# Optimization experiments

Measured on AMD Instinct MI355X. Metric: run time of the kernel, lower is better.

Reference implementation:

```python
import jax, jax.numpy as jnp
import numpy as np

N_EMBD = 2048
N_HEAD = 32
N_GROUPS = 8
HEAD_DIM = N_EMBD // N_HEAD
Q_PER_KV = N_HEAD // N_GROUPS
QKV_DIM = (Q_PER_KV + 2) * N_GROUPS * HEAD_DIM


def apply_rope(x, cos, sin):
    # x: [B, nH, T, hd]; cos/sin: [T, rot//2]
    B, nH, T, hd = x.shape
    rot = min(sin.shape[1] * 2, hd)
    half = rot // 2
    x_rot, x_pass = x[..., :rot], x[..., rot:]
    c = cos[:T, :half][None, None]  # [1,1,T,half]
    s = sin[:T, :half][None, None]
    x1, x2 = x_rot[..., :half], x_rot[..., half:]
    x1_ = x1 * c - x2 * s
    x2_ = x2 * c + x1 * s
    return jnp.concatenate([x1_, x2_, x_pass], axis=-1)


def setup_inputs() -> dict:
    key = jax.random.key(0)
    k1, k2, k3, k4, k5 = jax.random.split(key, 5)
    B, T = 2, 2048
    x = jax.random.normal(k1, (B, T, N_EMBD), dtype=jnp.float32)
    cos = jax.random.uniform(k2, (T, HEAD_DIM // 2), dtype=jnp.float32)
    sin = jax.random.uniform(k3, (T, HEAD_DIM // 2), dtype=jnp.float32)
    attn_w = jax.random.normal(k4, (QKV_DIM, N_EMBD), dtype=jnp.float32) * (1.0 / np.sqrt(N_EMBD))
    proj_w = jax.random.normal(k5, (N_EMBD, N_EMBD), dtype=jnp.float32) * (1.0 / np.sqrt(N_EMBD))
    return {"x": x, "cos": cos, "sin": sin, "attn_w": attn_w, "proj_w": proj_w}


def reference(x, cos, sin, attn_w, proj_w):
    B, T, E = x.shape
    qkv = jnp.einsum('bte,fe->btf', x, attn_w)  # [B,T,QKV_DIM]
    qkv = qkv.reshape(B, T, N_GROUPS, Q_PER_KV + 2, HEAD_DIM)
    q = qkv[:, :, :, :Q_PER_KV].reshape(B, T, N_HEAD, HEAD_DIM)
    k = qkv[:, :, :, Q_PER_KV]      # [B,T,G,hd]
    v = qkv[:, :, :, Q_PER_KV + 1]  # [B,T,G,hd]
    # [B, heads, T, hd] layout; GQA repeat_interleave of K/V to full head count
    q = q.transpose(0, 2, 1, 3)
    k = jnp.repeat(k.transpose(0, 2, 1, 3), Q_PER_KV, axis=1)
    v = jnp.repeat(v.transpose(0, 2, 1, 3), Q_PER_KV, axis=1)
    q = apply_rope(q, cos, sin)
    k = apply_rope(k, cos, sin)
    scale = 1.0 / np.sqrt(HEAD_DIM)
    att = jax.nn.softmax(jnp.einsum('bhqd,bhkd->bhqk', q, k) * scale, axis=-1)
    out = jnp.einsum('bhqk,bhkd->bhqd', att, v)  # [B,nH,T,hd]
    out = out.transpose(0, 2, 1, 3).reshape(B, T, N_HEAD * HEAD_DIM)
    return jnp.einsum('bte,fe->btf', out, proj_w)
```

## Files before the change

### kernel.cpp

```cpp
#include <hip/hip_runtime.h>

typedef unsigned short u16;
typedef unsigned int u32;
typedef __bf16 bf16x8 __attribute__((ext_vector_type(8)));
typedef float f32x4 __attribute__((ext_vector_type(4)));
typedef float f32x16 __attribute__((ext_vector_type(16)));
typedef unsigned int u32x4 __attribute__((ext_vector_type(4)));

__device__ __forceinline__ u16 f2bf(float f) {
    u32 u = __builtin_bit_cast(u32, f);
    u32 r = u + 0x7FFFu + ((u >> 16) & 1u);
    return (u16)(r >> 16);
}
__device__ __forceinline__ u32 pack_bf16(float v0, float v1) {
    u32 a = __builtin_bit_cast(u32, v0) + 0x8000u;
    u32 b = __builtin_bit_cast(u32, v1) + 0x8000u;
    return __builtin_amdgcn_perm(b, a, 0x07060302u);
}
__device__ __forceinline__ u32 cvtpk(float lo, float hi) {
    u32 r;
    asm("v_cvt_pk_bf16_f32 %0, %1, %2" : "=v"(r) : "v"(lo), "v"(hi));
    return r;
}
__device__ __forceinline__ void plswap(u32& a, u32& b) {
    asm("v_permlane32_swap_b32 %0, %1" : "+v"(a), "+v"(b));
}
__device__ __forceinline__ void gload16(const u16* g, u16* l) {
    __builtin_amdgcn_global_load_lds(
        (const __attribute__((address_space(1))) u32*)g,
        (__attribute__((address_space(3))) u32*)l, 16, 0, 0);
}

#define QSCALE 0.18033688011111793f


__global__ __launch_bounds__(256) void cvt3_kernel(const float* __restrict__ a, u16* __restrict__ ao,
                                                   const float* __restrict__ b, u16* __restrict__ bo,
                                                   const float* __restrict__ c, u16* __restrict__ co) {
    int i = blockIdx.x * 256 + threadIdx.x;
    const float* src; u16* dst; int idx;
    if (i < 2097152)       { src = a; dst = ao; idx = i; }
    else if (i < 3670016)  { src = b; dst = bo; idx = i - 2097152; }
    else                   { src = c; dst = co; idx = i - 3670016; }
    float4 f = reinterpret_cast<const float4*>(src)[idx];
    u32 lo = (u32)f2bf(f.x) | ((u32)f2bf(f.y) << 16);
    u32 hi = (u32)f2bf(f.z) | ((u32)f2bf(f.w) << 16);
    reinterpret_cast<uint2*>(dst)[idx] = make_uint2(lo, hi);
}

__global__ __launch_bounds__(512, 2) void gemm_qkv(const u16* __restrict__ A,
                                                   const u16* __restrict__ Bw,
                                                   const float* __restrict__ cosb,
                                                   const float* __restrict__ sinb,
                                                   u16* __restrict__ Qo,
                                                   u16* __restrict__ Ko,
                                                   u16* __restrict__ Vt) {
    __shared__ __align__(16) u16 As[2 * 2 * 128 * 64];
    __shared__ __align__(16) u16 Bs[2 * 2 * 128 * 64];
    const int tid = threadIdx.x;
    const int w = tid >> 6, lane = tid & 63;
    const int quad = lane >> 4, l15 = lane & 15;
    const int wr = w >> 2, wc = w & 3;
    const int m0 = blockIdx.x * 256, n0 = blockIdx.y * 256;
    const int K = 2048;
    const int rsub = lane >> 3;
    const int csrc = (lane & 7) ^ rsub;
    const int sx = (l15 & 7) << 3;
    const int c0 = (quad * 8) ^ sx;
    const int c1 = (32 + quad * 8) ^ sx;

    f32x4 acc[8][4];
#pragma unroll
    for (int a = 0; a < 8; a++)
#pragma unroll
        for (int b = 0; b < 4; b++) acc[a][b] = (f32x4){0.f, 0.f, 0.f, 0.f};

    auto stage = [&](const u16* g, int row0, int kk, u16* lds) {
#pragma unroll
        for (int i = 0; i < 2; i++)
            gload16(g + (size_t)(row0 + (i * 8 + w) * 8 + rsub) * K + kk + csrc * 8,
                    lds + (i * 8 + w) * 512);
    };

    stage(A,  m0,       0, &As[0]);
    stage(A,  m0 + 128, 0, &As[8192]);
    stage(Bw, n0,       0, &Bs[0]);
    stage(Bw, n0 + 128, 0, &Bs[8192]);
    asm volatile("s_waitcnt vmcnt(0)" ::: "memory");
    __builtin_amdgcn_s_barrier();

    for (int j = 0; j < 32; ++j) {
        const int cur = j & 1;
        const u16* Ab = &As[cur * 16384 + wr * 8192];
        const u16* Bb = &Bs[cur * 16384 + (wc >> 1) * 8192 + (wc & 1) * 4096];
        u16* Asn = &As[(cur ^ 1) * 16384];
        u16* Bsn = &Bs[(cur ^ 1) * 16384];
        const int kk2 = (j + 1) * 64;
        bf16x8 af[4][2];
#pragma unroll
        for (int q = 0; q < 4; ++q) {
            const int qm = q >> 1, qn = q & 1;
            if (qn == 0) {
#pragma unroll
                for (int fm = 0; fm < 4; fm++) {
                    af[fm][0] = *reinterpret_cast<const bf16x8*>(&Ab[(qm * 64 + fm * 16 + l15) * 64 + c0]);
                    af[fm][1] = *reinterpret_cast<const bf16x8*>(&Ab[(qm * 64 + fm * 16 + l15) * 64 + c1]);
                }
            }
            bf16x8 bfv[2][2];
#pragma unroll
            for (int fn = 0; fn < 2; fn++) {
                bfv[fn][0] = *reinterpret_cast<const bf16x8*>(&Bb[(qn * 32 + fn * 16 + l15) * 64 + c0]);
                bfv[fn][1] = *reinterpret_cast<const bf16x8*>(&Bb[(qn * 32 + fn * 16 + l15) * 64 + c1]);
            }
            if (j < 31) {
                if (q == 0)      { stage(A,  m0,       kk2, Asn); stage(A,  m0 + 128, kk2, Asn + 8192); }
                else if (q == 1) { stage(Bw, n0,       kk2, Bsn); stage(Bw, n0 + 128, kk2, Bsn + 8192); }
            }
            __builtin_amdgcn_s_barrier();
            __builtin_amdgcn_s_setprio(1);
#pragma unroll
            for (int fm = 0; fm < 4; fm++)
#pragma unroll
                for (int fn = 0; fn < 2; fn++) {
                    acc[qm * 4 + fm][qn * 2 + fn] = __builtin_amdgcn_mfma_f32_16x16x32_bf16(
                        af[fm][0], bfv[fn][0], acc[qm * 4 + fm][qn * 2 + fn], 0, 0, 0);
                    acc[qm * 4 + fm][qn * 2 + fn] = __builtin_amdgcn_mfma_f32_16x16x32_bf16(
                        af[fm][1], bfv[fn][1], acc[qm * 4 + fm][qn * 2 + fn], 0, 0, 0);
                }
            __builtin_amdgcn_s_setprio(0);
            if (q == 3 && j < 31) asm volatile("s_waitcnt vmcnt(0)" ::: "memory");
            __builtin_amdgcn_s_barrier();
        }
    }

    const int nw0 = n0 + wc * 64;
    const int G = nw0 / 384;
    const int slot = (nw0 % 384) / 64;
    const int bb = m0 >> 11;
    const int tb0 = (m0 & 2047) + wr * 128 + quad * 4;
    if (slot == 5) {
        u16* vbase = Vt + ((size_t)(bb * 8 + G)) * 131072;
        const int half_v = quad >> 1, jb = (quad & 1) * 4;
#pragma unroll
        for (int fm = 0; fm < 8; fm++) {
            const int trow = tb0 + fm * 16;
            const int sb = (trow >> 6) * 4096 + ((trow >> 4) & 3) * 512 + half_v * 256 + jb;
#pragma unroll
            for (int fn = 0; fn < 4; fn++) {
                const int dt = fn >> 1, dl = (fn & 1) * 16 + l15;
                uint2 pk;
                pk.x = pack_bf16(acc[fm][fn][0], acc[fm][fn][1]);
                pk.y = pack_bf16(acc[fm][fn][2], acc[fm][fn][3]);
                *reinterpret_cast<uint2*>(vbase + sb + dt * 2048 + dl * 8) = pk;
            }
        }
    } else {
        const float sc = (slot < 4) ? QSCALE : 1.0f;
        u16* obase = (slot < 4)
            ? Qo + ((size_t)(bb * 32 + G * 4 + slot)) * 131072
            : Ko + ((size_t)(bb * 8 + G)) * 131072;
        const int laneoff = (l15 >> 3) * 256 + (l15 & 7);
#pragma unroll
        for (int fm = 0; fm < 8; fm++) {
#pragma unroll
            for (int i = 0; i < 4; i++) {
                const int t = tb0 + fm * 16 + i;
                const int tb = (t >> 5) * 2048 + (t & 31) * 8 + laneoff;
#pragma unroll
                for (int fn = 0; fn < 2; fn++) {
                    const int dh = fn * 16 + l15;
                    float c = cosb[t * 32 + dh], s = sinb[t * 32 + dh];
                    float x1 = acc[fm][fn][i], x2 = acc[fm][fn + 2][i];
                    obase[tb + fn * 512]       = f2bf((x1 * c - x2 * s) * sc);
                    obase[tb + (fn + 2) * 512] = f2bf((x2 * c + x1 * s) * sc);
                }
            }
        }
    }
}

__global__ __launch_bounds__(256) void gemm_bt(const u16* __restrict__ A,
                                               const u16* __restrict__ Bw,
                                               float* __restrict__ Cf,
                                               int M, int N, int K) {
    __shared__ __align__(16) u16 As[2 * 128 * 32];
    __shared__ __align__(16) u16 Bs[2 * 128 * 32];
    const int tid = threadIdx.x;
    const int wave = tid >> 6, lane = tid & 63, quad = lane >> 4, l15 = lane & 15;
    const int wm = wave >> 1, wn = wave & 1;
    const int m0 = blockIdx.x * 128, n0 = blockIdx.y * 128;
    const int lrow = lane >> 2, lcol = (lane & 3) * 8;
    f32x4 acc[4][4];
#pragma unroll
    for (int a = 0; a < 4; a++)
#pragma unroll
        for (int b = 0; b < 4; b++) acc[a][b] = (f32x4){0.f, 0.f, 0.f, 0.f};
    for (int kk = 0; kk < K; kk += 64) {
        __syncthreads();
#pragma unroll
        for (int p = 0; p < 2; p++)
#pragma unroll
            for (int c = 0; c < 2; c++) {
                const int rA = wave * 32 + c * 16;
                gload16(A  + (size_t)(m0 + rA + lrow) * K + kk + p * 32 + lcol,
                        &As[p * 4096 + rA * 32]);
                gload16(Bw + (size_t)(n0 + rA + lrow) * K + kk + p * 32 + lcol,
                        &Bs[p * 4096 + rA * 32]);
            }
        __syncthreads();
#pragma unroll
        for (int p = 0; p < 2; p++) {
            bf16x8 af[4], bfr[4];
#pragma unroll
            for (int t = 0; t < 4; t++) {
                af[t]  = *reinterpret_cast<const bf16x8*>(
                    &As[p * 4096 + (wm * 64 + t * 16 + l15) * 32 + quad * 8]);
                bfr[t] = *reinterpret_cast<const bf16x8*>(
                    &Bs[p * 4096 + (wn * 64 + t * 16 + l15) * 32 + quad * 8]);
            }
#pragma unroll
            for (int tm = 0; tm < 4; tm++)
#pragma unroll
                for (int tn = 0; tn < 4; tn++)
                    acc[tm][tn] = __builtin_amdgcn_mfma_f32_16x16x32_bf16(af[tm], bfr[tn], acc[tm][tn], 0, 0, 0);
        }
    }
#pragma unroll
    for (int tm = 0; tm < 4; tm++) {
        const int r0 = m0 + wm * 64 + tm * 16 + quad * 4;
#pragma unroll
        for (int tn = 0; tn < 4; tn++) {
            const int c = n0 + wn * 64 + tn * 16 + l15;
#pragma unroll
            for (int i = 0; i < 4; i++) Cf[(size_t)(r0 + i) * N + c] = acc[tm][tn][i];
        }
    }
}

__global__ __launch_bounds__(256, 4) void attn(const u16* __restrict__ Q,
                                               const u16* __restrict__ Kg,
                                               const u16* __restrict__ Vt,
                                               u16* __restrict__ O) {
    __shared__ __align__(16) u16 Ks[2 * 4096];
    __shared__ __align__(16) u16 Vts[2 * 4096];
    const int tid = threadIdx.x, w = tid >> 6, lane = tid & 63;
    const int half = lane >> 5, l31 = lane & 31;
    const int q0 = blockIdx.x * 128;
    const int h = blockIdx.y, b = blockIdx.z, g = h >> 2;
    const u16* qfb = Q + ((size_t)(b * 32 + h)) * 131072;
    const u16* kfb = Kg + ((size_t)(b * 8 + g)) * 131072;
    const u16* vfb = Vt + ((size_t)(b * 8 + g)) * 131072;

    const int Tq = (q0 >> 6) + (w >> 1);
#pragma unroll
    for (int ks = 0; ks < 4; ks++)
        gload16(qfb + ((size_t)((Tq * 8 + (w & 1) * 4 + ks) * 64) + lane) * 8,
                Ks + (w * 4 + ks) * 512);
    __syncthreads();
    bf16x8 qf[4];
#pragma unroll
    for (int ks = 0; ks < 4; ks++)
        qf[ks] = *reinterpret_cast<const bf16x8*>(&Ks[(w * 4 + ks) * 512 + lane * 8]);
    __syncthreads();

    f32x16 Oa[2];
#pragma unroll
    for (int t = 0; t < 2; t++)
#pragma unroll
        for (int i = 0; i < 16; i++) Oa[t][i] = 0.f;
    float lsum = 0.f;

    auto stage_kv = [&](int T, int bsel) {
        u16* kd = Ks + bsel * 4096;
        u16* vd = Vts + bsel * 4096;
#pragma unroll
        for (int i = 0; i < 2; i++) {
            const int s = w * 2 + i;
            gload16(kfb + ((size_t)((T * 8 + s) * 64) + lane) * 8, kd + s * 512);
            gload16(vfb + ((size_t)((T * 8 + s) * 64) + lane) * 8, vd + s * 512);
        }
    };

    stage_kv(0, 0);
    __syncthreads();

    for (int t = 0; t < 32; t++) {
        if (t < 31) stage_kv(t + 1, (t + 1) & 1);
        const u16* Kb = Ks + (t & 1) * 4096;
        const u16* Vb = Vts + (t & 1) * 4096;

        float ps = 0.f;
        u32 pw[4][4];
#pragma unroll
        for (int kt = 0; kt < 2; kt++) {
            f32x16 S;
#pragma unroll
            for (int i = 0; i < 16; i++) S[i] = 0.f;
            __builtin_amdgcn_s_setprio(1);
#pragma unroll
            for (int ks = 0; ks < 4; ks++) {
                bf16x8 kf = *reinterpret_cast<const bf16x8*>(
                    &Kb[(kt * 4 + ks) * 512 + lane * 8]);
                S = __builtin_amdgcn_mfma_f32_32x32x16_bf16(kf, qf[ks], S, 0, 0, 0);
            }
            __builtin_amdgcn_s_setprio(0);
            float pe[16];
#pragma unroll
            for (int r = 0; r < 16; r++) pe[r] = __builtin_amdgcn_exp2f(S[r]);
#pragma unroll
            for (int r = 0; r < 4; r++)
                ps += (pe[r * 4 + 0] + pe[r * 4 + 1]) + (pe[r * 4 + 2] + pe[r * 4 + 3]);
#pragma unroll
            for (int j = 0; j < 2; j++) {
                u32 X0 = cvtpk(pe[j * 8 + 0], pe[j * 8 + 1]);
                u32 Y0 = cvtpk(pe[j * 8 + 4], pe[j * 8 + 5]);
                u32 X1 = cvtpk(pe[j * 8 + 2], pe[j * 8 + 3]);
                u32 Y1 = cvtpk(pe[j * 8 + 6], pe[j * 8 + 7]);
                plswap(X0, Y0);
                plswap(X1, Y1);
                const int ks2 = kt * 2 + j;
                pw[ks2][0] = X0; pw[ks2][1] = X1; pw[ks2][2] = Y0; pw[ks2][3] = Y1;
            }
        }
        lsum += ps;
        __builtin_amdgcn_s_setprio(1);
#pragma unroll
        for (int ks2 = 0; ks2 < 4; ks2++) {
            u32x4 pv = (u32x4){pw[ks2][0], pw[ks2][1], pw[ks2][2], pw[ks2][3]};
            bf16x8 pf = __builtin_bit_cast(bf16x8, pv);
#pragma unroll
            for (int dt = 0; dt < 2; dt++) {
                bf16x8 vf = *reinterpret_cast<const bf16x8*>(
                    &Vb[(dt * 4 + ks2) * 512 + lane * 8]);
                Oa[dt] = __builtin_amdgcn_mfma_f32_32x32x16_bf16(vf, pf, Oa[dt], 0, 0, 0);
            }
        }
        __builtin_amdgcn_s_setprio(0);
        __syncthreads();
    }
    float lt = lsum + __shfl_xor(lsum, 32);
    float linv = 1.f / lt;
    const int t = q0 + w * 32 + l31;
    u16* orow = O + ((size_t)(b * 2048 + t)) * 2048 + h * 64;
#pragma unroll
    for (int dt = 0; dt < 2; dt++)
#pragma unroll
        for (int gr = 0; gr < 4; gr++) {
            uint2 pk;
            pk.x = pack_bf16(Oa[dt][gr * 4 + 0] * linv, Oa[dt][gr * 4 + 1] * linv);
            pk.y = pack_bf16(Oa[dt][gr * 4 + 2] * linv, Oa[dt][gr * 4 + 3] * linv);
            *reinterpret_cast<uint2*>(orow + dt * 32 + 8 * gr + 4 * half) = pk;
        }
}

extern "C" void kernel_launch(void* const* d_in, const int* in_sizes, int n_in,
                              void* d_out, int out_size, void* d_ws, size_t ws_size,
                              hipStream_t stream) {
    const float* x      = (const float*)d_in[0];
    const float* cosb   = (const float*)d_in[1];
    const float* sinb   = (const float*)d_in[2];
    const float* attn_w = (const float*)d_in[3];
    const float* proj_w = (const float*)d_in[4];
    float* out = (float*)d_out;

    u16* xb  = (u16*)d_ws;
    u16* w1b = xb  + (size_t)4096 * 2048;
    u16* w2b = w1b + (size_t)3072 * 2048;
    u16* qo  = w2b + (size_t)2048 * 2048;
    u16* ko  = qo  + (size_t)2 * 32 * 2048 * 64;
    u16* vt  = ko  + (size_t)2 * 8 * 2048 * 64;
    u16* ao  = xb;

    cvt3_kernel<<<18432, 256, 0, stream>>>(x, xb, attn_w, w1b, proj_w, w2b);
    gemm_qkv<<<dim3(16, 12), 512, 0, stream>>>(xb, w1b, cosb, sinb, qo, ko, vt);
    attn<<<dim3(16, 32, 2), 256, 0, stream>>>(qo, ko, vt, ao);
    gemm_bt<<<dim3(32, 16), 256, 0, stream>>>(ao, w2b, out, 4096, 2048, 2048);
}
```

Baseline: 307.3 us.

## Software-pipeline QK^T one tile ahead with triple-buffered K in attention

```diff
diff --git a/kernel.cpp b/kernel.cpp
--- a/kernel.cpp
+++ b/kernel.cpp
@@ -242,7 +242,7 @@
                                                const u16* __restrict__ Kg,
                                                const u16* __restrict__ Vt,
                                                u16* __restrict__ O) {
-    __shared__ __align__(16) u16 Ks[2 * 4096];
+    __shared__ __align__(16) u16 Ks[3 * 4096];
     __shared__ __align__(16) u16 Vts[2 * 4096];
     const int tid = threadIdx.x, w = tid >> 6, lane = tid & 63;
     const int half = lane >> 5, l31 = lane & 31;
@@ -271,43 +271,55 @@
         for (int i = 0; i < 16; i++) Oa[t][i] = 0.f;
     float lsum = 0.f;
 
-    auto stage_kv = [&](int T, int bsel) {
+    auto stage_k = [&](int T, int bsel) {
         u16* kd = Ks + bsel * 4096;
-        u16* vd = Vts + bsel * 4096;
 #pragma unroll
         for (int i = 0; i < 2; i++) {
             const int s = w * 2 + i;
             gload16(kfb + ((size_t)((T * 8 + s) * 64) + lane) * 8, kd + s * 512);
+        }
+    };
+    auto stage_v = [&](int T, int bsel) {
+        u16* vd = Vts + bsel * 4096;
+#pragma unroll
+        for (int i = 0; i < 2; i++) {
+            const int s = w * 2 + i;
             gload16(vfb + ((size_t)((T * 8 + s) * 64) + lane) * 8, vd + s * 512);
         }
     };
-
-    stage_kv(0, 0);
+    auto qk = [&](f32x16 (&S)[2], const u16* Kb) {
+#pragma unroll
+        for (int kt = 0; kt < 2; kt++) {
+#pragma unroll
+            for (int i = 0; i < 16; i++) S[kt][i] = 0.f;
+#pragma unroll
+            for (int ks = 0; ks < 4; ks++) {
+                bf16x8 kf = *reinterpret_cast<const bf16x8*>(&Kb[(kt * 4 + ks) * 512 + lane * 8]);
+                S[kt] = __builtin_amdgcn_mfma_f32_32x32x16_bf16(kf, qf[ks], S[kt], 0, 0, 0);
+            }
+        }
+    };
+
+    stage_k(0, 0);
+    stage_v(0, 0);
+    stage_k(1, 1);
     __syncthreads();
-
-    for (int t = 0; t < 32; t++) {
-        if (t < 31) stage_kv(t + 1, (t + 1) & 1);
-        const u16* Kb = Ks + (t & 1) * 4096;
-        const u16* Vb = Vts + (t & 1) * 4096;
-
+    f32x16 Sa[2], Sb[2];
+    __builtin_amdgcn_s_setprio(1);
+    qk(Sa, Ks);
+    __builtin_amdgcn_s_setprio(0);
+
+    auto body = [&](int t, int bn, int bs, f32x16 (&Sc)[2], f32x16 (&Sn)[2],
+                    const u16* Vb) {
+        if (t < 31) stage_v(t + 1, (t + 1) & 1);
+        if (t < 30) stage_k(t + 2, bs);
         float ps = 0.f;
         u32 pw[4][4];
 #pragma unroll
         for (int kt = 0; kt < 2; kt++) {
-            f32x16 S;
-#pragma unroll
-            for (int i = 0; i < 16; i++) S[i] = 0.f;
-            __builtin_amdgcn_s_setprio(1);
-#pragma unroll
-            for (int ks = 0; ks < 4; ks++) {
-                bf16x8 kf = *reinterpret_cast<const bf16x8*>(
-                    &Kb[(kt * 4 + ks) * 512 + lane * 8]);
-                S = __builtin_amdgcn_mfma_f32_32x32x16_bf16(kf, qf[ks], S, 0, 0, 0);
-            }
-            __builtin_amdgcn_s_setprio(0);
             float pe[16];
 #pragma unroll
-            for (int r = 0; r < 16; r++) pe[r] = __builtin_amdgcn_exp2f(S[r]);
+            for (int r = 0; r < 16; r++) pe[r] = __builtin_amdgcn_exp2f(Sc[kt][r]);
 #pragma unroll
             for (int r = 0; r < 4; r++)
                 ps += (pe[r * 4 + 0] + pe[r * 4 + 1]) + (pe[r * 4 + 2] + pe[r * 4 + 3]);
@@ -323,8 +335,8 @@
                 pw[ks2][0] = X0; pw[ks2][1] = X1; pw[ks2][2] = Y0; pw[ks2][3] = Y1;
             }
         }
-        lsum += ps;
         __builtin_amdgcn_s_setprio(1);
+        qk(Sn, Ks + bn * 4096);
 #pragma unroll
         for (int ks2 = 0; ks2 < 4; ks2++) {
             u32x4 pv = (u32x4){pw[ks2][0], pw[ks2][1], pw[ks2][2], pw[ks2][3]};
@@ -337,8 +349,19 @@
             }
         }
         __builtin_amdgcn_s_setprio(0);
+        lsum += ps;
         __syncthreads();
+    };
+
+    int b0 = 0, b1 = 1, b2 = 2;
+    for (int k2 = 0; k2 < 16; ++k2) {
+        const int t0 = k2 * 2;
+        body(t0,     b1, b2, Sa, Sb, Vts);
+        body(t0 + 1, b2, b0, Sb, Sa, Vts + 4096);
+        const int nb0 = b2, nb1 = b0, nb2 = b1;
+        b0 = nb0; b1 = nb1; b2 = nb2;
     }
+
     float lt = lsum + __shfl_xor(lsum, 32);
     float linv = 1.f / lt;
     const int t = q0 + w * 32 + l31;
```

Result: slower. 314.8 us (+2.4%).
